# Kernel tuning notes

Hardware: AMD Instinct MI355X
Metric: run time of the kernel (lower is better)

Reference implementation:

```python
import jax, jax.numpy as jnp
import numpy as np

N, F, H, C = 50000, 128, 4, 32  # nodes, in-features, heads, per-head dim
E = 800000
D = H * C  # concat output dim = 128


def _tconv(x, src, dst, ea, Wq, bq, Wk, bk, Wv, bv, We, Ws, bs):
    # PyG TransformerConv (concat=True, root_weight=True, beta=False, eval mode)
    n = x.shape[0]
    q = (x @ Wq + bq).reshape(n, H, C)
    k = (x @ Wk + bk).reshape(n, H, C)
    v = (x @ Wv + bv).reshape(n, H, C)
    e = (ea @ We).reshape(-1, H, C)            # edge embedding [E,H,C]
    kj = k[src] + e                            # gathered keys + edge emb
    alpha = jnp.einsum('ehc,ehc->eh', q[dst], kj) / jnp.sqrt(jnp.float32(C))
    amax = jax.ops.segment_max(alpha, dst, num_segments=n)
    ex = jnp.exp(alpha - amax[dst])
    denom = jax.ops.segment_sum(ex, dst, num_segments=n)
    w = ex / (denom[dst] + 1e-16)              # segment softmax over in-edges
    msg = (v[src] + e) * w[:, :, None]
    out = jax.ops.segment_sum(msg, dst, num_segments=n).reshape(n, D)
    return out + x @ Ws + bs                   # skip connection


def setup_inputs() -> dict:
    key = jax.random.key(0)
    ks = jax.random.split(key, 24)
    s = lambda i, shape, scale: jax.random.normal(ks[i], shape, dtype=jnp.float32) * scale
    inp = {
        'x': s(0, (N, F), 1.0),
        'edge_index': jax.random.randint(ks[1], (2, E), 0, N),
        'edge_attr': s(2, (E,), 1.0),
        # layer 1 (in = F)
        'Wq1': s(3, (F, D), 1.0 / np.sqrt(F)), 'bq1': jnp.zeros((D,), jnp.float32),
        'Wk1': s(4, (F, D), 1.0 / np.sqrt(F)), 'bk1': jnp.zeros((D,), jnp.float32),
        'Wv1': s(5, (F, D), 1.0 / np.sqrt(F)), 'bv1': jnp.zeros((D,), jnp.float32),
        'We1': s(6, (1, D), 1.0),
        'Ws1': s(7, (F, D), 1.0 / np.sqrt(F)), 'bs1': jnp.zeros((D,), jnp.float32),
        # layer 2 (in = D)
        'Wq2': s(8, (D, D), 1.0 / np.sqrt(D)), 'bq2': jnp.zeros((D,), jnp.float32),
        'Wk2': s(9, (D, D), 1.0 / np.sqrt(D)), 'bk2': jnp.zeros((D,), jnp.float32),
        'Wv2': s(10, (D, D), 1.0 / np.sqrt(D)), 'bv2': jnp.zeros((D,), jnp.float32),
        'We2': s(11, (1, D), 1.0),
        'Ws2': s(12, (D, D), 1.0 / np.sqrt(D)), 'bs2': jnp.zeros((D,), jnp.float32),
    }
    return inp


def reference(x, edge_index, edge_attr,
              Wq1, bq1, Wk1, bk1, Wv1, bv1, We1, Ws1, bs1,
              Wq2, bq2, Wk2, bk2, Wv2, bv2, We2, Ws2, bs2):
    src, dst = edge_index[0], edge_index[1]
    ea = edge_attr.reshape(-1, 1)
    h = _tconv(x, src, dst, ea, Wq1, bq1, Wk1, bk1, Wv1, bv1, We1, Ws1, bs1)
    h = jax.nn.relu(h)  # dropout is identity in eval mode
    h = _tconv(h, src, dst, ea, Wq2, bq2, Wk2, bk2, Wv2, bv2, We2, Ws2, bs2)
    return jax.nn.relu(h)
```

## Files before the change

### kernel.cpp

```cpp
#include <hip/hip_runtime.h>


#define TPB 256

typedef __attribute__((ext_vector_type(8))) short short8v;
typedef __attribute__((ext_vector_type(8))) unsigned short ushort8v;
typedef __attribute__((ext_vector_type(16))) float f32x16;

__device__ __forceinline__ unsigned short f2bf(float f) {
    unsigned u = __float_as_uint(f);
    u = (u + 0x7FFFu + ((u >> 16) & 1u)) >> 16;
    return (unsigned short)u;
}
__device__ __forceinline__ float bf2f(unsigned short s) {
    return __uint_as_float((unsigned)s << 16);
}
__device__ __forceinline__ float exp2_hw(float x) {
    float r;
    asm("v_exp_f32 %0, %1" : "=v"(r) : "v"(x));
    return r;
}

__global__ void __launch_bounds__(TPB) prep_cvt_k(
    const float* __restrict__ Wq1, const float* __restrict__ Wk1,
    const float* __restrict__ Wv1, const float* __restrict__ Ws1,
    const float* __restrict__ Wq2, const float* __restrict__ Wk2,
    const float* __restrict__ Wv2, const float* __restrict__ Ws2,
    unsigned short* __restrict__ pack,
    const float* __restrict__ x, unsigned short* __restrict__ xb, int n4)
{
    if (blockIdx.x < 512) {
        int i = blockIdx.x * TPB + threadIdx.x;
        int j = i & 7, lane = (i >> 3) & 63, t = (i >> 9) & 7, nc = (i >> 12) & 3, g = (i >> 14) & 7;
        const float* Wt[8] = {Wq1, Wk1, Wv1, Ws1, Wq2, Wk2, Wv2, Ws2};
        const float* W = Wt[g];
        int kk = t * 16 + (lane >> 5) * 8 + j;
        int nn = nc * 32 + (lane & 31);
        pack[i] = f2bf(W[kk * 128 + nn]);
    } else {
        int i = (blockIdx.x - 512) * TPB + threadIdx.x;
        if (i >= n4) return;
        float4 v = *(const float4*)(x + (size_t)i * 4);
        ushort4 o;
        o.x = f2bf(v.x); o.y = f2bf(v.y); o.z = f2bf(v.z); o.w = f2bf(v.w);
        *(ushort4*)(xb + (size_t)i * 4) = o;
    }
}

__global__ void __launch_bounds__(TPB) gemm_mfma_k(
    const unsigned short* __restrict__ A, int M,
    const unsigned short* __restrict__ pack,
    const float* __restrict__ bq, const float* __restrict__ bk,
    const float* __restrict__ bv, const float* __restrict__ bs,
    unsigned short* __restrict__ oq, unsigned short* __restrict__ okv,
    float* __restrict__ os)
{
    const int g = blockIdx.y;
    const int row0 = blockIdx.x * 128;
    const int wv = threadIdx.x >> 6;
    const int lane = threadIdx.x & 63;
    const int rbase = row0 + wv * 32;
    const int arow = rbase + (lane & 31);
    const int kh = (lane >> 5) * 8;

    const short8v z8 = {0, 0, 0, 0, 0, 0, 0, 0};
    short8v a[8];
    if (arow < M) {
        const unsigned short* Ap = A + (size_t)arow * 128 + kh;
#pragma unroll
        for (int t = 0; t < 8; ++t) a[t] = *(const short8v*)(Ap + t * 16);
    } else {
#pragma unroll
        for (int t = 0; t < 8; ++t) a[t] = z8;
    }

    f32x16 acc[4];
#pragma unroll
    for (int nc = 0; nc < 4; ++nc)
#pragma unroll
        for (int r = 0; r < 16; ++r) acc[nc][r] = 0.f;

    const unsigned short* bp = pack + (size_t)g * 16384;
#pragma unroll
    for (int nc = 0; nc < 4; ++nc) {
#pragma unroll
        for (int t = 0; t < 8; ++t) {
            short8v b = *(const short8v*)(bp + (nc * 8 + t) * 512 + lane * 8);
            acc[nc] = __builtin_amdgcn_mfma_f32_32x32x16_bf16(a[t], b, acc[nc], 0, 0, 0);
        }
    }

    const float* bias = g == 0 ? bq : (g == 1 ? bk : (g == 2 ? bv : bs));
    const int col = lane & 31;
    const int rb2 = rbase + 4 * (lane >> 5);
    if (g == 3) {
#pragma unroll
        for (int nc = 0; nc < 4; ++nc) {
            float bb = bias[nc * 32 + col];
#pragma unroll
            for (int r = 0; r < 16; ++r) {
                int row = rb2 + (r & 3) + 8 * (r >> 2);
                if (row < M) os[(size_t)row * 128 + nc * 32 + col] = acc[nc][r] + bb;
            }
        }
    } else {
        unsigned short* out = g == 0 ? oq : okv;
        const int stride = g == 0 ? 128 : 256;
        const int goff = g == 2 ? 128 : 0;
#pragma unroll
        for (int nc = 0; nc < 4; ++nc) {
            float bb = bias[nc * 32 + col];
#pragma unroll
            for (int r = 0; r < 16; ++r) {
                int row = rb2 + (r & 3) + 8 * (r >> 2);
                if (row < M)
                    out[(size_t)row * stride + goff + nc * 32 + col] = f2bf(acc[nc][r] + bb);
            }
        }
    }
}

__global__ void __launch_bounds__(TPB) hist_k(const int* __restrict__ dst,
                                              int* __restrict__ deg, int E)
{
    int e = blockIdx.x * TPB + threadIdx.x;
    if (e < E) atomicAdd(&deg[dst[e]], 1);
}

__global__ void __launch_bounds__(TPB) scan_a_k(const int* __restrict__ deg, int n,
                                                int* __restrict__ incl,
                                                int* __restrict__ bsum,
                                                int* __restrict__ bcnt, int nb,
                                                int* __restrict__ rank)
{
    __shared__ int ts[TPB];
    __shared__ int lhist[64];
    if (threadIdx.x < 64) lhist[threadIdx.x] = 0;
    const int base = blockIdx.x * 1024;
    int vals[4], s = 0;
#pragma unroll
    for (int j = 0; j < 4; ++j) {
        int i = base + threadIdx.x * 4 + j;
        vals[j] = (i < n) ? deg[i] : 0;
        s += vals[j];
    }
    ts[threadIdx.x] = s;
    __syncthreads();
#pragma unroll
    for (int j = 0; j < 4; ++j) {
        int i = base + threadIdx.x * 4 + j;
        if (i < n) {
            int bin = 63 - min(vals[j], 63);
            rank[i] = atomicAdd(&lhist[bin], 1);
        }
    }
    for (int off = 1; off < TPB; off <<= 1) {
        int u = (threadIdx.x >= off) ? ts[threadIdx.x - off] : 0;
        __syncthreads();
        ts[threadIdx.x] += u;
        __syncthreads();
    }
    int run = ts[threadIdx.x] - s;
#pragma unroll
    for (int j = 0; j < 4; ++j) {
        run += vals[j];
        int i = base + threadIdx.x * 4 + j;
        if (i < n) incl[i] = run;
    }
    if (threadIdx.x == TPB - 1) bsum[blockIdx.x] = ts[TPB - 1];
    __syncthreads();
    if (threadIdx.x < 64) bcnt[threadIdx.x * nb + blockIdx.x] = lhist[threadIdx.x];
}

__global__ void __launch_bounds__(TPB) scan_b_k(int* __restrict__ bsum, int nb,
                                                int* __restrict__ bcnt)
{
    __shared__ int ts[TPB];
    const int t = threadIdx.x;
    int v = (t < nb) ? bsum[t] : 0;
    ts[t] = v;
    __syncthreads();
    for (int off = 1; off < TPB; off <<= 1) {
        int u = (t >= off) ? ts[t - off] : 0;
        __syncthreads();
        ts[t] += u;
        __syncthreads();
    }
    if (t < nb) bsum[t] = ts[t] - v;
    __syncthreads();

    const int total = 64 * nb;
    const int C = (total + TPB - 1) / TPB;
    int loc[32];
    int s = 0;
    for (int j = 0; j < C; ++j) {
        int i = t * C + j;
        loc[j] = (i < total) ? bcnt[i] : 0;
        s += loc[j];
    }
    __syncthreads();
    ts[t] = s;
    __syncthreads();
    for (int off = 1; off < TPB; off <<= 1) {
        int u = (t >= off) ? ts[t - off] : 0;
        __syncthreads();
        ts[t] += u;
        __syncthreads();
    }
    int run = ts[t] - s;
    for (int j = 0; j < C; ++j) {
        int i = t * C + j;
        if (i < total) bcnt[i] = run;
        run += loc[j];
    }
}

__global__ void __launch_bounds__(TPB) finalize_k(const int* __restrict__ incl,
                                                  const int* __restrict__ deg,
                                                  const int* __restrict__ bsum, int n,
                                                  int* __restrict__ row_ptr,
                                                  int* __restrict__ cursor,
                                                  const int* __restrict__ bcnt, int nb,
                                                  const int* __restrict__ rank,
                                                  int* __restrict__ perm)
{
    const int base = blockIdx.x * 1024;
    const int boff = bsum[blockIdx.x];
#pragma unroll
    for (int j = 0; j < 4; ++j) {
        int i = base + threadIdx.x * 4 + j;
        if (i < n) {
            int dg = deg[i];
            int iv = incl[i] + boff;
            row_ptr[i] = iv - dg;
            cursor[i] = iv - dg;
            if (i == n - 1) row_ptr[n] = iv;
            int bin = 63 - min(dg, 63);
            perm[bcnt[bin * nb + blockIdx.x] + rank[i]] = i;
        }
    }
}

__global__ void __launch_bounds__(TPB) scatter_k(
    const int* __restrict__ src, const int* __restrict__ dst,
    const float* __restrict__ ea, int* __restrict__ cursor,
    unsigned* __restrict__ csr_pack, int E)
{
    int e = blockIdx.x * TPB + threadIdx.x;
    if (e >= E) return;
    int pos = atomicAdd(&cursor[dst[e]], 1);
    csr_pack[pos] = ((unsigned)f2bf(ea[e]) << 16) | (unsigned)src[e];
}

template <bool BF16OUT>
__global__ void __launch_bounds__(TPB) node_attn_k(
    const unsigned short* __restrict__ q, const unsigned short* __restrict__ kv,
    const float* __restrict__ skip, const float* __restrict__ We,
    const int* __restrict__ row_ptr, const unsigned* __restrict__ csr_pack,
    const int* __restrict__ perm,
    void* __restrict__ outp, int n)
{
    const int slot = blockIdx.x * 16 + (threadIdx.x >> 4);
    if (slot >= n) return;
    const int node = perm[slot];
    const int l16 = threadIdx.x & 15;
    const int c8 = l16 * 8;

    const float C2 = 0.17677669529663687f * 1.44269504088896f;

    float we8[8], qv[8];
    {
        float4 wlo = *(const float4*)(We + c8);
        float4 whi = *(const float4*)(We + c8 + 4);
        we8[0] = wlo.x; we8[1] = wlo.y; we8[2] = wlo.z; we8[3] = wlo.w;
        we8[4] = whi.x; we8[5] = whi.y; we8[6] = whi.z; we8[7] = whi.w;
        ushort8v qu = *(const ushort8v*)(q + (size_t)node * 128 + c8);
#pragma unroll
        for (int i = 0; i < 8; ++i) qv[i] = bf2f((unsigned short)qu[i]) * C2;
    }

    float qwe = 0.f;
#pragma unroll
    for (int i = 0; i < 8; ++i) qwe = fmaf(qv[i], we8[i], qwe);
    qwe += __shfl_xor(qwe, 1);
    qwe += __shfl_xor(qwe, 2);

    const int p0 = row_ptr[node], p1 = row_ptr[node + 1];

    float m = -3.4e38f, l = 0.f, sae = 0.f;
    float acc[8];
#pragma unroll
    for (int i = 0; i < 8; ++i) acc[i] = 0.f;

    for (int j = p0; j < p1; j += 4) {
        const int last = p1 - 1;
        unsigned pr0 = csr_pack[j];
        unsigned pr1 = csr_pack[min(j + 1, last)];
        unsigned pr2 = csr_pack[min(j + 2, last)];
        unsigned pr3 = csr_pack[min(j + 3, last)];
        const unsigned short* b0 = kv + (pr0 & 0xFFFFu) * 256u + c8;
        const unsigned short* b1 = kv + (pr1 & 0xFFFFu) * 256u + c8;
        const unsigned short* b2 = kv + (pr2 & 0xFFFFu) * 256u + c8;
        const unsigned short* b3 = kv + (pr3 & 0xFFFFu) * 256u + c8;
        ushort8v ku0 = *(const ushort8v*)b0;
        ushort8v ku1 = *(const ushort8v*)b1;
        ushort8v ku2 = *(const ushort8v*)b2;
        ushort8v ku3 = *(const ushort8v*)b3;
        ushort8v vu0 = *(const ushort8v*)(b0 + 128);
        ushort8v vu1 = *(const ushort8v*)(b1 + 128);
        ushort8v vu2 = *(const ushort8v*)(b2 + 128);
        ushort8v vu3 = *(const ushort8v*)(b3 + 128);

        float d0 = 0.f, d1 = 0.f, d2 = 0.f, d3 = 0.f;
#pragma unroll
        for (int i = 0; i < 8; ++i) {
            d0 = fmaf(bf2f((unsigned short)ku0[i]), qv[i], d0);
            d1 = fmaf(bf2f((unsigned short)ku1[i]), qv[i], d1);
            d2 = fmaf(bf2f((unsigned short)ku2[i]), qv[i], d2);
            d3 = fmaf(bf2f((unsigned short)ku3[i]), qv[i], d3);
        }
        d0 += __shfl_xor(d0, 1); d0 += __shfl_xor(d0, 2);
        d1 += __shfl_xor(d1, 1); d1 += __shfl_xor(d1, 2);
        d2 += __shfl_xor(d2, 1); d2 += __shfl_xor(d2, 2);
        d3 += __shfl_xor(d3, 1); d3 += __shfl_xor(d3, 2);

        float ea0 = bf2f((unsigned short)(pr0 >> 16));
        float ea1 = bf2f((unsigned short)(pr1 >> 16));
        float ea2 = bf2f((unsigned short)(pr2 >> 16));
        float ea3 = bf2f((unsigned short)(pr3 >> 16));
        float al0 = fmaf(ea0, qwe, d0);
        float al1 = (j + 1 < p1) ? fmaf(ea1, qwe, d1) : -3.4e38f;
        float al2 = (j + 2 < p1) ? fmaf(ea2, qwe, d2) : -3.4e38f;
        float al3 = (j + 3 < p1) ? fmaf(ea3, qwe, d3) : -3.4e38f;

        float mn = fmaxf(m, fmaxf(fmaxf(al0, al1), fmaxf(al2, al3)));
        float sc = exp2_hw(m - mn);
        float pe0 = exp2_hw(al0 - mn), pe1 = exp2_hw(al1 - mn);
        float pe2 = exp2_hw(al2 - mn), pe3 = exp2_hw(al3 - mn);

        l = fmaf(l, sc, (pe0 + pe1) + (pe2 + pe3));
        sae = fmaf(sae, sc, fmaf(pe3, ea3, fmaf(pe2, ea2, fmaf(pe1, ea1, pe0 * ea0))));
#pragma unroll
        for (int i = 0; i < 8; ++i) {
            float mv = fmaf(pe0, bf2f((unsigned short)vu0[i]),
                       fmaf(pe1, bf2f((unsigned short)vu1[i]),
                       fmaf(pe2, bf2f((unsigned short)vu2[i]),
                            pe3 * bf2f((unsigned short)vu3[i]))));
            acc[i] = fmaf(acc[i], sc, mv);
        }
        m = mn;
    }

    float inv = 1.f / (l + 1e-16f);
    float4 sklo = *(const float4*)(skip + (size_t)node * 128 + c8);
    float4 skhi = *(const float4*)(skip + (size_t)node * 128 + c8 + 4);
    float sk[8] = {sklo.x, sklo.y, sklo.z, sklo.w, skhi.x, skhi.y, skhi.z, skhi.w};
    float o[8];
#pragma unroll
    for (int i = 0; i < 8; ++i)
        o[i] = fmaxf(fmaf(fmaf(sae, we8[i], acc[i]), inv, sk[i]), 0.f);

    if (BF16OUT) {
        ushort8v ov;
#pragma unroll
        for (int i = 0; i < 8; ++i) ov[i] = f2bf(o[i]);
        *(ushort8v*)((unsigned short*)outp + (size_t)node * 128 + c8) = ov;
    } else {
        float* op = (float*)outp + (size_t)node * 128 + c8;
        *(float4*)op = make_float4(o[0], o[1], o[2], o[3]);
        *(float4*)(op + 4) = make_float4(o[4], o[5], o[6], o[7]);
    }
}

extern "C" void kernel_launch(void* const* d_in, const int* in_sizes, int n_in,
                              void* d_out, int out_size, void* d_ws, size_t ws_size,
                              hipStream_t stream)
{
    const float* x   = (const float*)d_in[0];
    const int*   ei  = (const int*)d_in[1];
    const float* ea  = (const float*)d_in[2];
    const float* Wq1 = (const float*)d_in[3];  const float* bq1 = (const float*)d_in[4];
    const float* Wk1 = (const float*)d_in[5];  const float* bk1 = (const float*)d_in[6];
    const float* Wv1 = (const float*)d_in[7];  const float* bv1 = (const float*)d_in[8];
    const float* We1 = (const float*)d_in[9];
    const float* Ws1 = (const float*)d_in[10]; const float* bs1 = (const float*)d_in[11];
    const float* Wq2 = (const float*)d_in[12]; const float* bq2 = (const float*)d_in[13];
    const float* Wk2 = (const float*)d_in[14]; const float* bk2 = (const float*)d_in[15];
    const float* Wv2 = (const float*)d_in[16]; const float* bv2 = (const float*)d_in[17];
    const float* We2 = (const float*)d_in[18];
    const float* Ws2 = (const float*)d_in[19]; const float* bs2 = (const float*)d_in[20];

    const int N = in_sizes[0] / 128;
    const int E = in_sizes[1] / 2;
    const int* src = ei;
    const int* dst = ei + E;
    float* outf = (float*)d_out;

    const int nb = (N + 1023) / 1024;

    unsigned short* q  = (unsigned short*)d_ws;
    unsigned short* kv = q + (size_t)N * 128;
    float*          s  = (float*)(kv + (size_t)N * 256);
    unsigned short* xb = (unsigned short*)(s + (size_t)N * 128);
    unsigned short* pk = xb + (size_t)N * 128;
    int*   row_ptr = (int*)(pk + 131072);
    int*   deg     = row_ptr + (N + 1);
    int*   incl    = deg + N;
    int*   cursor  = incl + N;
    int*   rank    = cursor + N;
    int*   bsum    = rank + N;
    int*   bcnt    = bsum + 256;
    int*   perm    = bcnt + 64 * nb;
    unsigned* csr_pack = (unsigned*)(perm + N);

    const int gE   = (E + TPB - 1) / TPB;
    const int gN16 = (N + 15) / 16;
    const int n4   = N * 128 / 4;
    const int gPC  = 512 + (n4 + TPB - 1) / TPB;
    const int gG   = (N + 127) / 128;
    const dim3 gGd(gG, 4);

    hipMemsetAsync(deg, 0, (size_t)N * sizeof(int), stream);
    hist_k<<<gE, TPB, 0, stream>>>(dst, deg, E);
    scan_a_k<<<nb, TPB, 0, stream>>>(deg, N, incl, bsum, bcnt, nb, rank);
    scan_b_k<<<1, TPB, 0, stream>>>(bsum, nb, bcnt);
    finalize_k<<<nb, TPB, 0, stream>>>(incl, deg, bsum, N, row_ptr, cursor,
                                       bcnt, nb, rank, perm);
    scatter_k<<<gE, TPB, 0, stream>>>(src, dst, ea, cursor, csr_pack, E);

    prep_cvt_k<<<gPC, TPB, 0, stream>>>(Wq1, Wk1, Wv1, Ws1, Wq2, Wk2, Wv2, Ws2,
                                        pk, x, xb, n4);

    gemm_mfma_k<<<gGd, TPB, 0, stream>>>(xb, N, pk, bq1, bk1, bv1, bs1, q, kv, s);
    node_attn_k<true><<<gN16, TPB, 0, stream>>>(q, kv, s, We1, row_ptr, csr_pack,
                                                perm, xb, N);
    gemm_mfma_k<<<gGd, TPB, 0, stream>>>(xb, N, pk + 65536, bq2, bk2, bv2, bs2,
                                         q, kv, s);
    node_attn_k<false><<<gN16, TPB, 0, stream>>>(q, kv, s, We2, row_ptr, csr_pack,
                                                 perm, outf, N);
}
```

Before: 324.7 us.

## Store skip projection in bf16 and unroll attention edge loop to eight

The skip-connection GEMM output is now written as bf16 instead of fp32, which halves the skip write in the GEMM and the skip read in the attention kernel. The per-node online-softmax loop now handles eight edges per iteration instead of four, so more independent K/V gathers are in flight to hide latency. The costs are more registers per thread, which may lower occupancy, more wasted work on padded edges for low-degree nodes, and a small loss of precision in the skip term.

```diff
diff --git a/kernel.cpp b/kernel.cpp
--- a/kernel.cpp
+++ b/kernel.cpp
@@ -53,7 +53,7 @@
     const float* __restrict__ bq, const float* __restrict__ bk,
     const float* __restrict__ bv, const float* __restrict__ bs,
     unsigned short* __restrict__ oq, unsigned short* __restrict__ okv,
-    float* __restrict__ os)
+    unsigned short* __restrict__ os)
 {
     const int g = blockIdx.y;
     const int row0 = blockIdx.x * 128;
@@ -93,29 +93,17 @@
     const float* bias = g == 0 ? bq : (g == 1 ? bk : (g == 2 ? bv : bs));
     const int col = lane & 31;
     const int rb2 = rbase + 4 * (lane >> 5);
-    if (g == 3) {
-#pragma unroll
-        for (int nc = 0; nc < 4; ++nc) {
-            float bb = bias[nc * 32 + col];
-#pragma unroll
-            for (int r = 0; r < 16; ++r) {
-                int row = rb2 + (r & 3) + 8 * (r >> 2);
-                if (row < M) os[(size_t)row * 128 + nc * 32 + col] = acc[nc][r] + bb;
-            }
-        }
-    } else {
-        unsigned short* out = g == 0 ? oq : okv;
-        const int stride = g == 0 ? 128 : 256;
-        const int goff = g == 2 ? 128 : 0;
-#pragma unroll
-        for (int nc = 0; nc < 4; ++nc) {
-            float bb = bias[nc * 32 + col];
-#pragma unroll
-            for (int r = 0; r < 16; ++r) {
-                int row = rb2 + (r & 3) + 8 * (r >> 2);
-                if (row < M)
-                    out[(size_t)row * stride + goff + nc * 32 + col] = f2bf(acc[nc][r] + bb);
-            }
+    unsigned short* out = g == 0 ? oq : (g == 3 ? os : okv);
+    const int stride = (g == 1 || g == 2) ? 256 : 128;
+    const int goff = g == 2 ? 128 : 0;
+#pragma unroll
+    for (int nc = 0; nc < 4; ++nc) {
+        float bb = bias[nc * 32 + col];
+#pragma unroll
+        for (int r = 0; r < 16; ++r) {
+            int row = rb2 + (r & 3) + 8 * (r >> 2);
+            if (row < M)
+                out[(size_t)row * stride + goff + nc * 32 + col] = f2bf(acc[nc][r] + bb);
         }
     }
 }
@@ -255,7 +243,7 @@
 template <bool BF16OUT>
 __global__ void __launch_bounds__(TPB) node_attn_k(
     const unsigned short* __restrict__ q, const unsigned short* __restrict__ kv,
-    const float* __restrict__ skip, const float* __restrict__ We,
+    const unsigned short* __restrict__ skip, const float* __restrict__ We,
     const int* __restrict__ row_ptr, const unsigned* __restrict__ csr_pack,
     const int* __restrict__ perm,
     void* __restrict__ outp, int n)
@@ -292,73 +280,70 @@
 #pragma unroll
     for (int i = 0; i < 8; ++i) acc[i] = 0.f;
 
-    for (int j = p0; j < p1; j += 4) {
+    for (int j = p0; j < p1; j += 8) {
         const int last = p1 - 1;
-        unsigned pr0 = csr_pack[j];
-        unsigned pr1 = csr_pack[min(j + 1, last)];
-        unsigned pr2 = csr_pack[min(j + 2, last)];
-        unsigned pr3 = csr_pack[min(j + 3, last)];
-        const unsigned short* b0 = kv + (pr0 & 0xFFFFu) * 256u + c8;
-        const unsigned short* b1 = kv + (pr1 & 0xFFFFu) * 256u + c8;
-        const unsigned short* b2 = kv + (pr2 & 0xFFFFu) * 256u + c8;
-        const unsigned short* b3 = kv + (pr3 & 0xFFFFu) * 256u + c8;
-        ushort8v ku0 = *(const ushort8v*)b0;
-        ushort8v ku1 = *(const ushort8v*)b1;
-        ushort8v ku2 = *(const ushort8v*)b2;
-        ushort8v ku3 = *(const ushort8v*)b3;
-        ushort8v vu0 = *(const ushort8v*)(b0 + 128);
-        ushort8v vu1 = *(const ushort8v*)(b1 + 128);
-        ushort8v vu2 = *(const ushort8v*)(b2 + 128);
-        ushort8v vu3 = *(const ushort8v*)(b3 + 128);
-
-        float d0 = 0.f, d1 = 0.f, d2 = 0.f, d3 = 0.f;
+        unsigned pr[8];
+#pragma unroll
+        for (int t = 0; t < 8; ++t) pr[t] = csr_pack[min(j + t, last)];
+
+        ushort8v ku[8], vu[8];
+#pragma unroll
+        for (int t = 0; t < 8; ++t) {
+            const unsigned short* b = kv + (pr[t] & 0xFFFFu) * 256u + c8;
+            ku[t] = *(const ushort8v*)b;
+            vu[t] = *(const ushort8v*)(b + 128);
+        }
+
+        float d[8];
+#pragma unroll
+        for (int t = 0; t < 8; ++t) {
+            float dd = 0.f;
+#pragma unroll
+            for (int i = 0; i < 8; ++i)
+                dd = fmaf(bf2f((unsigned short)ku[t][i]), qv[i], dd);
+            dd += __shfl_xor(dd, 1);
+            dd += __shfl_xor(dd, 2);
+            d[t] = dd;
+        }
+
+        float eav[8], al[8];
+#pragma unroll
+        for (int t = 0; t < 8; ++t) {
+            eav[t] = bf2f((unsigned short)(pr[t] >> 16));
+            al[t] = (t == 0 || j + t < p1) ? fmaf(eav[t], qwe, d[t]) : -3.4e38f;
+        }
+
+        float mn = m;
+#pragma unroll
+        for (int t = 0; t < 8; ++t) mn = fmaxf(mn, al[t]);
+        float sc = exp2_hw(m - mn);
+        float pe[8];
+#pragma unroll
+        for (int t = 0; t < 8; ++t) pe[t] = exp2_hw(al[t] - mn);
+
+        float ls = 0.f, ss = 0.f;
+#pragma unroll
+        for (int t = 0; t < 8; ++t) { ls += pe[t]; ss = fmaf(pe[t], eav[t], ss); }
+        l = fmaf(l, sc, ls);
+        sae = fmaf(sae, sc, ss);
 #pragma unroll
         for (int i = 0; i < 8; ++i) {
-            d0 = fmaf(bf2f((unsigned short)ku0[i]), qv[i], d0);
-            d1 = fmaf(bf2f((unsigned short)ku1[i]), qv[i], d1);
-            d2 = fmaf(bf2f((unsigned short)ku2[i]), qv[i], d2);
-            d3 = fmaf(bf2f((unsigned short)ku3[i]), qv[i], d3);
-        }
-        d0 += __shfl_xor(d0, 1); d0 += __shfl_xor(d0, 2);
-        d1 += __shfl_xor(d1, 1); d1 += __shfl_xor(d1, 2);
-        d2 += __shfl_xor(d2, 1); d2 += __shfl_xor(d2, 2);
-        d3 += __shfl_xor(d3, 1); d3 += __shfl_xor(d3, 2);
-
-        float ea0 = bf2f((unsigned short)(pr0 >> 16));
-        float ea1 = bf2f((unsigned short)(pr1 >> 16));
-        float ea2 = bf2f((unsigned short)(pr2 >> 16));
-        float ea3 = bf2f((unsigned short)(pr3 >> 16));
-        float al0 = fmaf(ea0, qwe, d0);
-        float al1 = (j + 1 < p1) ? fmaf(ea1, qwe, d1) : -3.4e38f;
-        float al2 = (j + 2 < p1) ? fmaf(ea2, qwe, d2) : -3.4e38f;
-        float al3 = (j + 3 < p1) ? fmaf(ea3, qwe, d3) : -3.4e38f;
-
-        float mn = fmaxf(m, fmaxf(fmaxf(al0, al1), fmaxf(al2, al3)));
-        float sc = exp2_hw(m - mn);
-        float pe0 = exp2_hw(al0 - mn), pe1 = exp2_hw(al1 - mn);
-        float pe2 = exp2_hw(al2 - mn), pe3 = exp2_hw(al3 - mn);
-
-        l = fmaf(l, sc, (pe0 + pe1) + (pe2 + pe3));
-        sae = fmaf(sae, sc, fmaf(pe3, ea3, fmaf(pe2, ea2, fmaf(pe1, ea1, pe0 * ea0))));
-#pragma unroll
-        for (int i = 0; i < 8; ++i) {
-            float mv = fmaf(pe0, bf2f((unsigned short)vu0[i]),
-                       fmaf(pe1, bf2f((unsigned short)vu1[i]),
-                       fmaf(pe2, bf2f((unsigned short)vu2[i]),
-                            pe3 * bf2f((unsigned short)vu3[i]))));
+            float mv = 0.f;
+#pragma unroll
+            for (int t = 0; t < 8; ++t)
+                mv = fmaf(pe[t], bf2f((unsigned short)vu[t][i]), mv);
             acc[i] = fmaf(acc[i], sc, mv);
         }
         m = mn;
     }
 
     float inv = 1.f / (l + 1e-16f);
-    float4 sklo = *(const float4*)(skip + (size_t)node * 128 + c8);
-    float4 skhi = *(const float4*)(skip + (size_t)node * 128 + c8 + 4);
-    float sk[8] = {sklo.x, sklo.y, sklo.z, sklo.w, skhi.x, skhi.y, skhi.z, skhi.w};
+    ushort8v sku = *(const ushort8v*)(skip + (size_t)node * 128 + c8);
     float o[8];
 #pragma unroll
     for (int i = 0; i < 8; ++i)
-        o[i] = fmaxf(fmaf(fmaf(sae, we8[i], acc[i]), inv, sk[i]), 0.f);
+        o[i] = fmaxf(fmaf(fmaf(sae, we8[i], acc[i]), inv,
+                          bf2f((unsigned short)sku[i])), 0.f);
 
     if (BF16OUT) {
         ushort8v ov;
@@ -400,8 +385,8 @@
 
     unsigned short* q  = (unsigned short*)d_ws;
     unsigned short* kv = q + (size_t)N * 128;
-    float*          s  = (float*)(kv + (size_t)N * 256);
-    unsigned short* xb = (unsigned short*)(s + (size_t)N * 128);
+    unsigned short* s  = kv + (size_t)N * 256;
+    unsigned short* xb = s + (size_t)N * 128;
     unsigned short* pk = xb + (size_t)N * 128;
     int*   row_ptr = (int*)(pk + 131072);
     int*   deg     = row_ptr + (N + 1);
```

After: 303.0 us. -6.7%, faster.
